# Kernel optimization log

Hardware: AMD Instinct MI355X
Metric: run time of the kernel (lower is better)

Reference implementation:

```python
import jax, jax.numpy as jnp
import numpy as np


def _knn_gather(x, idx):
    # x: (B,N,D), idx: (B,N,K) -> (B,N,K,D)
    return jax.vmap(lambda xb, ib: xb[ib])(x, idx)


def _frames_and_knn(points, k):
    # brute-force self-KNN (ascending distance; idx[...,0] == self point)
    d2 = jnp.sum(points * points, -1)
    dist = d2[:, :, None] - 2.0 * jnp.einsum('bnd,bmd->bnm', points, points) + d2[:, None, :]
    _, idx = jax.lax.top_k(-dist, k)
    knn = _knn_gather(points, idx)                       # (B,N,K,3)
    cent = knn - knn.mean(-2, keepdims=True)
    # NOTE: original divides by shape[-1]-1 == 2 (coordinate dim), faithful to source
    covs = jnp.einsum('bnki,bnkj->bnij', cent, cent) / 2.0
    _, evecs = jnp.linalg.eigh(covs)
    frames = jnp.swapaxes(evecs, -1, -2)                 # rows = eigvecs, ascending eigval
    det = jnp.linalg.det(frames)                         # det of frames BEFORE modification
    frames = frames.at[:, :, 1, :].multiply(det[..., None])
    return idx, knn, frames


def reference(points, k, local_W):
    B, N, _ = points.shape
    idx, knn, frames = _frames_and_knn(points, k)
    diff = knn - points[:, :, None, :]                   # (B,N,K,3)
    normals = frames[:, :, 0, :]
    t1 = frames[:, :, 1, :]
    t2 = frames[:, :, 2, :]
    dt = jnp.stack([jnp.einsum('bnkd,bnd->bnk', diff, t1),
                    jnp.einsum('bnkd,bnd->bnk', diff, t2)], -1)  # (B,N,K,2)

    # ---- local Voronoi area via tangent-plane grid (nested KNN, K=1) ----
    rescale = 1.1
    bbox_min = dt.min(-2) * rescale                      # (B,N,2)
    bbox_max = dt.max(-2) * rescale
    max_len = (bbox_max - bbox_min).max(-1)              # (B,N)
    coords = (dt - bbox_min[:, :, None, :]) / max_len[:, :, None, None] * 2.0 - 1.0

    lin = jnp.linspace(-1.0, 1.0, local_W, dtype=points.dtype)
    X, Y = jnp.meshgrid(lin, lin, indexing='ij')
    grid = jnp.stack([X, Y], -1).reshape(-1, 2)          # (G,2), G = local_W**2

    CHUNK = 128
    c = coords.reshape(-1, k, 2)
    n_pts = c.shape[0]
    pad = (-n_pts) % CHUNK
    c = jnp.pad(c, ((0, pad), (0, 0), (0, 0)))

    def count_fn(cc):                                    # cc: (CHUNK,K,2)
        d = jnp.sum((grid[None, :, None, :] - cc[:, None, :, :]) ** 2, -1)  # (CHUNK,G,K)
        return jnp.sum(jnp.argmin(d, -1) == 0, -1)       # grid cells owned by center

    counts = jax.lax.map(count_fn, c.reshape(-1, CHUNK, k, 2)).reshape(-1)[:n_pts]
    counts = counts.reshape(B, N).astype(points.dtype)
    voronoi_area = counts * max_len ** 2 / (local_W - 1) ** 2    # (B,N)

    # ---- Weingarten fields / Gaussian curvature ----
    ln = _knn_gather(normals, idx) - normals[:, :, None, :]      # (B,N,K,3)
    dn = jnp.stack([jnp.einsum('bnkd,bnd->bnk', ln, t1),
                    jnp.einsum('bnkd,bnd->bnk', ln, t2)], -1)    # (B,N,K,2)
    XXT = jnp.einsum('bnki,bnkj->bnij', dt, dt)                  # (B,N,2,2)
    YXT = jnp.einsum('bnki,bnkj->bnij', dn, dt)
    S = YXT + jnp.swapaxes(YXT, -1, -2)                          # YXT + XYT
    w, Q = jnp.linalg.eigh(XXT)
    QTSQ = jnp.einsum('bnji,bnjk,bnkl->bnil', Q, S, Q)           # Q^T S Q
    a, b = w[..., 0], w[..., 1]
    cmat = jnp.stack([jnp.stack([2 * a, a + b], -1),
                      jnp.stack([a + b, 2 * b], -1)], -2)        # (B,N,2,2)
    E = QTSQ / (cmat + 1e-8)
    Wmap = jnp.einsum('bnij,bnjk,bnlk->bnil', Q, E, Q)           # Q E Q^T
    gauss = jnp.linalg.det(Wmap)                                 # (B,N)

    euler = jnp.sum(gauss.reshape(-1) * voronoi_area.reshape(-1)) / 2.0 / jnp.pi
    return euler


def setup_inputs() -> dict:
    key = jax.random.key(0)
    points = jax.random.normal(key, (1, 4096, 3), dtype=jnp.float32)
    return {"points": points, "k": 50, "local_W": 64}
```

## Files before the change

kernel.cpp:

```cpp
#include <hip/hip_runtime.h>
#include <math.h>

#define NPTS 4096
#define KNB  50
#define WGRID 64

__device__ int   g_idx[NPTS * KNB];
__device__ float g_dt[NPTS * KNB * 2];
__device__ float g_nrm[NPTS * 3];
__device__ float g_t1[NPTS * 3];
__device__ float g_t2[NPTS * 3];
__device__ float g_bmin[NPTS * 2];
__device__ float g_ml[NPTS];
__device__ float g_va[NPTS];

__device__ __forceinline__ float slapy2f(float x, float y) {
  float ax = fabsf(x), ay = fabsf(y);
  float w = fmaxf(ax, ay), z = fminf(ax, ay);
  if (z == 0.0f) return w;
  float t = z / w;
  return w * sqrtf(1.0f + t * t);
}

__device__ __forceinline__ void slartgf(float f, float g, float* cs, float* sn, float* r) {
  const float safmin = 1.1754944e-38f;
  const float safmax = 8.5070592e+37f;
  const float rtmin = 1.0842022e-19f;
  const float rtmax = 6.5219496e+18f;
  if (g == 0.0f) {
    *cs = 1.0f; *sn = 0.0f; *r = f;
  } else if (f == 0.0f) {
    *cs = 0.0f; *sn = copysignf(1.0f, g); *r = fabsf(g);
  } else {
    float f1 = fabsf(f), g1 = fabsf(g);
    if (f1 > rtmin && f1 < rtmax && g1 > rtmin && g1 < rtmax) {
      float d = sqrtf(f * f + g * g);
      float p = 1.0f / d;
      *cs = f1 * p;
      *sn = g * copysignf(p, f);
      *r = copysignf(d, f);
    } else {
      float u = fminf(safmax, fmaxf(safmin, fmaxf(f1, g1)));
      float fs = f / u, gs = g / u;
      float d = sqrtf(fs * fs + gs * gs);
      float p = 1.0f / d;
      *cs = fabsf(fs) * p;
      *sn = gs * copysignf(p, f);
      *r = copysignf(d, f) * u;
    }
  }
}

__device__ void slaev2f(float a, float b, float c, float* rt1, float* rt2,
                        float* cs1, float* sn1) {
  float sm = a + c;
  float df = a - c;
  float adf = fabsf(df);
  float tb = b + b;
  float ab = fabsf(tb);
  float acmx, acmn;
  if (fabsf(a) > fabsf(c)) { acmx = a; acmn = c; } else { acmx = c; acmn = a; }
  float rt;
  if (adf > ab)      { float t = ab / adf; rt = adf * sqrtf(1.0f + t * t); }
  else if (adf < ab) { float t = adf / ab; rt = ab * sqrtf(1.0f + t * t); }
  else               { rt = ab * sqrtf(2.0f); }
  int sgn1;
  if (sm < 0.0f) {
    *rt1 = 0.5f * (sm - rt); sgn1 = -1;
    *rt2 = (acmx / *rt1) * acmn - (b / *rt1) * b;
  } else if (sm > 0.0f) {
    *rt1 = 0.5f * (sm + rt); sgn1 = 1;
    *rt2 = (acmx / *rt1) * acmn - (b / *rt1) * b;
  } else {
    *rt1 = 0.5f * rt; *rt2 = -0.5f * rt; sgn1 = 1;
  }
  float cs; int sgn2;
  if (df >= 0.0f) { cs = df + rt; sgn2 = 1; }
  else            { cs = df - rt; sgn2 = -1; }
  float acs = fabsf(cs);
  if (acs > ab) {
    float ct = -tb / cs;
    *sn1 = 1.0f / sqrtf(1.0f + ct * ct);
    *cs1 = ct * (*sn1);
  } else {
    if (ab == 0.0f) { *cs1 = 1.0f; *sn1 = 0.0f; }
    else {
      float tn = -cs / tb;
      *cs1 = 1.0f / sqrtf(1.0f + tn * tn);
      *sn1 = tn * (*cs1);
    }
  }
  if (sgn1 == sgn2) { float tn = *cs1; *cs1 = -(*sn1); *sn1 = tn; }
}

__device__ void ssteqr3(float* d, float* e, float Z[3][3]) {
  const float eps = 5.9604645e-08f;
  const float eps2 = 3.5527137e-15f;
  const float safmin = 1.1754944e-38f;
  const float ssfmax = 3.0744574e+18f;
  const float ssfmin = 3.0517578e-05f;
  const int n = 3, nmaxit = 90;
  int jtot = 0;
  for (int r = 0; r < 3; ++r)
    for (int c = 0; c < 3; ++c) Z[r][c] = (r == c) ? 1.0f : 0.0f;

  int l1 = 1;
  while (l1 <= n) {
    if (l1 > 1) e[l1 - 2] = 0.0f;
    int m = n;
    for (int mm = l1; mm <= n - 1; ++mm) {
      float tst = fabsf(e[mm - 1]);
      if (tst == 0.0f) { m = mm; break; }
      if (tst <= (sqrtf(fabsf(d[mm - 1])) * sqrtf(fabsf(d[mm]))) * eps) {
        e[mm - 1] = 0.0f; m = mm; break;
      }
    }
    int l = l1, lsv = l1, lend = m, lendsv = m;
    l1 = m + 1;
    if (lend == l) continue;

    float anorm = 0.0f;
    for (int ii = l; ii <= lend; ++ii) anorm = fmaxf(anorm, fabsf(d[ii - 1]));
    for (int ii = l; ii <= lend - 1; ++ii) anorm = fmaxf(anorm, fabsf(e[ii - 1]));
    if (anorm == 0.0f) continue;
    int iscale = 0;
    if (anorm > ssfmax) {
      iscale = 1; float mul = ssfmax / anorm;
      for (int ii = l; ii <= lend; ++ii) d[ii - 1] *= mul;
      for (int ii = l; ii <= lend - 1; ++ii) e[ii - 1] *= mul;
    } else if (anorm < ssfmin) {
      iscale = 2; float mul = ssfmin / anorm;
      for (int ii = l; ii <= lend; ++ii) d[ii - 1] *= mul;
      for (int ii = l; ii <= lend - 1; ++ii) e[ii - 1] *= mul;
    }
    if (fabsf(d[lend - 1]) < fabsf(d[l - 1])) { lend = lsv; l = lendsv; }

    if (lend > l) {
      for (;;) {
        int mm = lend;
        if (l != lend) {
          for (int t = l; t <= lend - 1; ++t) {
            float tst = e[t - 1] * e[t - 1];
            if (tst <= (eps2 * fabsf(d[t - 1])) * fabsf(d[t]) + safmin) { mm = t; break; }
          }
        }
        if (mm < lend) e[mm - 1] = 0.0f;
        float p = d[l - 1];
        if (mm == l) {
          d[l - 1] = p; ++l;
          if (l <= lend) continue; break;
        }
        if (mm == l + 1) {
          float rt1, rt2, c, s;
          slaev2f(d[l - 1], e[l - 1], d[l], &rt1, &rt2, &c, &s);
          for (int r = 0; r < 3; ++r) {
            float t = Z[r][l];
            Z[r][l]     = c * t - s * Z[r][l - 1];
            Z[r][l - 1] = s * t + c * Z[r][l - 1];
          }
          d[l - 1] = rt1; d[l] = rt2; e[l - 1] = 0.0f;
          l += 2;
          if (l <= lend) continue; break;
        }
        if (jtot == nmaxit) break;
        ++jtot;
        float g = (d[l] - p) / (2.0f * e[l - 1]);
        float r = slapy2f(g, 1.0f);
        g = d[mm - 1] - p + e[l - 1] / (g + copysignf(r, g));
        float s = 1.0f, c = 1.0f;
        p = 0.0f;
        float cw[2], sw[2];
        for (int i = mm - 1; i >= l; --i) {
          float f = s * e[i - 1];
          float b = c * e[i - 1];
          slartgf(g, f, &c, &s, &r);
          if (i != mm - 1) e[i] = r;
          g = d[i] - p;
          r = (d[i - 1] - g) * s + 2.0f * c * b;
          p = s * r;
          d[i] = g + p;
          g = c * r - b;
          cw[i - l] = c; sw[i - l] = -s;
        }
        for (int j = mm - 1; j >= l; --j) {
          float cc = cw[j - l], ss = sw[j - l];
          for (int r2 = 0; r2 < 3; ++r2) {
            float t = Z[r2][j];
            Z[r2][j]     = cc * t - ss * Z[r2][j - 1];
            Z[r2][j - 1] = ss * t + cc * Z[r2][j - 1];
          }
        }
        d[l - 1] -= p;
        e[l - 1] = g;
      }
    } else {
      for (;;) {
        int mm = lend;
        if (l != lend) {
          for (int t = l; t >= lend + 1; --t) {
            float tst = e[t - 2] * e[t - 2];
            if (tst <= (eps2 * fabsf(d[t - 1])) * fabsf(d[t - 2]) + safmin) { mm = t; break; }
          }
        }
        if (mm > lend) e[mm - 2] = 0.0f;
        float p = d[l - 1];
        if (mm == l) {
          d[l - 1] = p; --l;
          if (l >= lend) continue; break;
        }
        if (mm == l - 1) {
          float rt1, rt2, c, s;
          slaev2f(d[l - 2], e[l - 2], d[l - 1], &rt1, &rt2, &c, &s);
          for (int r2 = 0; r2 < 3; ++r2) {
            float t = Z[r2][l - 1];
            Z[r2][l - 1] = c * t - s * Z[r2][l - 2];
            Z[r2][l - 2] = s * t + c * Z[r2][l - 2];
          }
          d[l - 2] = rt1; d[l - 1] = rt2; e[l - 2] = 0.0f;
          l -= 2;
          if (l >= lend) continue; break;
        }
        if (jtot == nmaxit) break;
        ++jtot;
        float g = (d[l - 2] - p) / (2.0f * e[l - 2]);
        float r = slapy2f(g, 1.0f);
        g = d[mm - 1] - p + e[l - 2] / (g + copysignf(r, g));
        float s = 1.0f, c = 1.0f;
        p = 0.0f;
        float cw[2], sw[2];
        for (int i = mm; i <= l - 1; ++i) {
          float f = s * e[i - 1];
          float b = c * e[i - 1];
          slartgf(g, f, &c, &s, &r);
          if (i != mm) e[i - 2] = r;
          g = d[i - 1] - p;
          r = (d[i] - g) * s + 2.0f * c * b;
          p = s * r;
          d[i - 1] = g + p;
          g = c * r - b;
          cw[i - mm] = c; sw[i - mm] = s;
        }
        for (int j = mm; j <= l - 1; ++j) {
          float cc = cw[j - mm], ss = sw[j - mm];
          for (int r2 = 0; r2 < 3; ++r2) {
            float t = Z[r2][j];
            Z[r2][j]     = cc * t - ss * Z[r2][j - 1];
            Z[r2][j - 1] = ss * t + cc * Z[r2][j - 1];
          }
        }
        d[l - 1] -= p;
        e[l - 2] = g;
      }
    }
    if (iscale == 1) {
      float mul = anorm / ssfmax;
      for (int ii = lsv; ii <= lendsv; ++ii) d[ii - 1] *= mul;
      for (int ii = lsv; ii <= lendsv - 1; ++ii) e[ii - 1] *= mul;
    } else if (iscale == 2) {
      float mul = anorm / ssfmin;
      for (int ii = lsv; ii <= lendsv; ++ii) d[ii - 1] *= mul;
      for (int ii = lsv; ii <= lendsv - 1; ++ii) e[ii - 1] *= mul;
    }
    if (jtot >= nmaxit) break;
  }
  for (int ii = 2; ii <= n; ++ii) {
    int i0 = ii - 1, k0 = i0;
    float p = d[i0 - 1];
    for (int j = ii; j <= n; ++j)
      if (d[j - 1] < p) { k0 = j; p = d[j - 1]; }
    if (k0 != i0) {
      d[k0 - 1] = d[i0 - 1]; d[i0 - 1] = p;
      for (int r2 = 0; r2 < 3; ++r2) {
        float t = Z[r2][i0 - 1]; Z[r2][i0 - 1] = Z[r2][k0 - 1]; Z[r2][k0 - 1] = t;
      }
    }
  }
}

__device__ void ssytrd3(float a11, float a21, float a31, float a22, float a32, float a33,
                        float d[3], float e[2], float* tau, float* u) {
  float xnorm = fabsf(a31);
  if (xnorm == 0.0f) {
    *tau = 0.0f; *u = 0.0f;
    d[0] = a11; d[1] = a22; d[2] = a33; e[0] = a21; e[1] = a32;
    return;
  }
  float beta = -copysignf(slapy2f(a21, xnorm), a21);
  float taui = (beta - a21) / beta;
  float uu = a31 * (1.0f / (a21 - beta));
  float w1 = taui * a22 + taui * (a32 * uu);
  float w2 = taui * a32 + (taui * uu) * a33;
  float alpha = -0.5f * taui * (w1 + w2 * uu);
  w1 += alpha; w2 += alpha * uu;
  float na22 = a22 - 2.0f * w1;
  float na32 = a32 - (uu * w1 + w2);
  float na33 = a33 - 2.0f * (uu * w2);
  d[0] = a11; d[1] = na22; d[2] = na33;
  e[0] = beta; e[1] = na32;
  *tau = taui; *u = uu;
}

__global__ __launch_bounds__(256) void knn_kernel(const float* __restrict__ pts,
                                                  float* __restrict__ out, int N) {
  __shared__ unsigned skey[NPTS];
  __shared__ unsigned hist[256];
  __shared__ unsigned sred[4];
  __shared__ unsigned sbin[2];
  __shared__ int   eqi[64];
  __shared__ float eqd[64];
  __shared__ unsigned eqn[1];
  const int i = blockIdx.x;
  const int tid = threadIdx.x;
  const int lane = tid & 63, wid = tid >> 6;
  if (i == 0 && tid == 0) out[0] = 0.0f;
  const float xi = pts[3 * i], yi = pts[3 * i + 1], zi = pts[3 * i + 2];
  const float d2i = xi * xi + yi * yi + zi * zi;
  hist[tid] = 0;
  if (tid == 0) eqn[0] = 0;
  __syncthreads();
  for (int j = tid; j < N; j += 256) {
    float xj = pts[3 * j], yj = pts[3 * j + 1], zj = pts[3 * j + 2];
    float d2j = xj * xj + yj * yj + zj * zj;
    float dot = fmaf(zi, zj, fmaf(yi, yj, xi * xj));
    float dist = (d2i - 2.0f * dot) + d2j;
    float dc = fminf(fmaxf(dist, 0.0f), 31.0f);
    unsigned u = (unsigned)(dc * 134217728.0f);
    skey[j] = u;
    atomicAdd(&hist[u >> 24], 1u);
  }
  __syncthreads();
  unsigned prefix = 0, rank = 49;
  for (int pass = 0; pass < 2; ++pass) {
    const int shift = 24 - 8 * pass;
    if (pass) {
      for (int j = tid; j < N; j += 256) {
        unsigned u = skey[j];
        if ((u >> 24) == (prefix >> 24))
          atomicAdd(&hist[(u >> 16) & 255u], 1u);
      }
      __syncthreads();
    }
    unsigned h = hist[tid];
    unsigned c = h;
    #pragma unroll
    for (int off = 1; off < 64; off <<= 1) {
      unsigned o = __shfl_up(c, off);
      if (lane >= off) c += o;
    }
    if (lane == 63) sred[wid] = c;
    __syncthreads();
    unsigned wbase = 0;
    for (int w2 = 0; w2 < wid; ++w2) wbase += sred[w2];
    c += wbase;
    unsigned excl = c - h;
    if (rank >= excl && rank < c) { sbin[0] = (unsigned)tid; sbin[1] = rank - excl; }
    __syncthreads();
    prefix |= sbin[0] << shift;
    rank = sbin[1];
    __syncthreads();
    if (pass == 0) { hist[tid] = 0; __syncthreads(); }
  }
  const unsigned T = prefix;
  int cnt = 0;
  for (int j = tid; j < N; j += 256) {
    unsigned u = skey[j];
    if (u < T && j != i) {
      ++cnt;
    } else if ((u & 0xFFFF0000u) == T) {
      float xj = pts[3 * j], yj = pts[3 * j + 1], zj = pts[3 * j + 2];
      float d2j = xj * xj + yj * yj + zj * zj;
      float dot = fmaf(zi, zj, fmaf(yi, yj, xi * xj));
      float dist = (d2i - 2.0f * dot) + d2j;
      unsigned e = atomicAdd(&eqn[0], 1u);
      if (e < 64u) { eqi[e] = j; eqd[e] = dist; }
    }
  }
  __syncthreads();
  unsigned cc = (unsigned)cnt;
  #pragma unroll
  for (int off = 1; off < 64; off <<= 1) {
    unsigned o = __shfl_up(cc, off);
    if (lane >= off) cc += o;
  }
  if (lane == 63) sred[wid] = cc;
  __syncthreads();
  unsigned wbase = 0;
  for (int w2 = 0; w2 < wid; ++w2) wbase += sred[w2];
  int base = 1 + (int)(wbase + cc - (unsigned)cnt);
  for (int j = tid; j < N; j += 256) {
    unsigned u = skey[j];
    if (u < T && j != i) g_idx[i * KNB + (base++)] = j;
  }
  if (tid == 0) {
    g_idx[i * KNB] = i;
    int slot = 1 + (int)(sred[0] + sred[1] + sred[2] + sred[3]);
    int need = KNB - slot;
    int ne = (int)eqn[0]; if (ne > 64) ne = 64;
    for (int e2 = 0; e2 < need; ++e2) {
      int bq = 0, bidx = 0x7FFFFFFF; float bd = 3.4e38f;
      for (int q = 0; q < ne; ++q) {
        if (eqi[q] < 0) continue;
        float dq = eqd[q];
        if (dq < bd || (dq == bd && eqi[q] < bidx)) { bd = dq; bidx = eqi[q]; bq = q; }
      }
      g_idx[i * KNB + slot + e2] = bidx;
      eqi[bq] = -1;
    }
  }
}

__global__ __launch_bounds__(256) void frames_kernel(const float* __restrict__ pts, int N) {
  __shared__ float sx[4][52], sy[4][52], sz[4][52];
  const int tid = threadIdx.x, lane = tid & 63, w = tid >> 6;
  const int i = blockIdx.x * 4 + w;
  const int base = i * KNB;
  if (lane < KNB) {
    int j = g_idx[base + lane];
    sx[w][lane] = pts[3 * j];
    sy[w][lane] = pts[3 * j + 1];
    sz[w][lane] = pts[3 * j + 2];
  }
  __syncthreads();
  float mx = 0.0f, my = 0.0f, mz = 0.0f;
  for (int kk = 0; kk < KNB; ++kk) { mx += sx[w][kk]; my += sy[w][kk]; mz += sz[w][kk]; }
  mx /= 50.0f; my /= 50.0f; mz /= 50.0f;
  float c00 = 0, c01 = 0, c02 = 0, c11 = 0, c12 = 0, c22 = 0;
  for (int kk = 0; kk < KNB; ++kk) {
    float cx = sx[w][kk] - mx, cy = sy[w][kk] - my, cz = sz[w][kk] - mz;
    c00 = fmaf(cx, cx, c00); c01 = fmaf(cx, cy, c01); c02 = fmaf(cx, cz, c02);
    c11 = fmaf(cy, cy, c11); c12 = fmaf(cy, cz, c12); c22 = fmaf(cz, cz, c22);
  }
  c00 *= 0.5f; c01 *= 0.5f; c02 *= 0.5f; c11 *= 0.5f; c12 *= 0.5f; c22 *= 0.5f;

  float d[3], e[2], tau, u;
  ssytrd3(c00, c01, c02, c11, c12, c22, d, e, &tau, &u);
  float Z[3][3];
  ssteqr3(d, e, Z);
  if (tau != 0.0f) {
    for (int c = 0; c < 3; ++c) {
      float sum = Z[1][c] + u * Z[2][c];
      Z[1][c] -= tau * sum;
      Z[2][c] -= tau * u * sum;
    }
  }
  float n0 = Z[0][0], n1 = Z[1][0], n2 = Z[2][0];
  float a0 = Z[0][1], a1 = Z[1][1], a2 = Z[2][1];
  float b0 = Z[0][2], b1 = Z[1][2], b2 = Z[2][2];
  float cxp = a1 * b2 - a2 * b1, cyp = a2 * b0 - a0 * b2, czp = a0 * b1 - a1 * b0;
  float det = n0 * cxp + n1 * cyp + n2 * czp;
  a0 *= det; a1 *= det; a2 *= det;

  const float xi = pts[3 * i], yi = pts[3 * i + 1], zi = pts[3 * i + 2];
  float dt0 = 0.0f, dt1 = 0.0f;
  float mn0 = 3.0e38f, mx0 = -3.0e38f, mn1 = 3.0e38f, mx1 = -3.0e38f;
  if (lane < KNB) {
    float dx = sx[w][lane] - xi, dy = sy[w][lane] - yi, dz = sz[w][lane] - zi;
    dt0 = dx * a0 + dy * a1 + dz * a2;
    dt1 = dx * b0 + dy * b1 + dz * b2;
    g_dt[2 * (base + lane)] = dt0;
    g_dt[2 * (base + lane) + 1] = dt1;
    mn0 = dt0; mx0 = dt0; mn1 = dt1; mx1 = dt1;
  }
  #pragma unroll
  for (int off = 32; off > 0; off >>= 1) {
    mn0 = fminf(mn0, __shfl_down(mn0, off));
    mx0 = fmaxf(mx0, __shfl_down(mx0, off));
    mn1 = fminf(mn1, __shfl_down(mn1, off));
    mx1 = fmaxf(mx1, __shfl_down(mx1, off));
  }
  if (lane == 0) {
    g_nrm[3 * i] = n0; g_nrm[3 * i + 1] = n1; g_nrm[3 * i + 2] = n2;
    g_t1[3 * i] = a0;  g_t1[3 * i + 1] = a1;  g_t1[3 * i + 2] = a2;
    g_t2[3 * i] = b0;  g_t2[3 * i + 1] = b1;  g_t2[3 * i + 2] = b2;
    float bmin0 = mn0 * 1.1f, bmax0 = mx0 * 1.1f;
    float bmin1 = mn1 * 1.1f, bmax1 = mx1 * 1.1f;
    float ml = fmaxf(bmax0 - bmin0, bmax1 - bmin1);
    g_bmin[2 * i] = bmin0; g_bmin[2 * i + 1] = bmin1;
    g_ml[i] = ml;
  }
}

__global__ __launch_bounds__(256, 8) void voronoi_kernel(int N) {
  __shared__ float2 sc[KNB];
  __shared__ int alist[64];
  __shared__ int acnt[1];
  __shared__ int swc[4];
  const int i = blockIdx.x;
  const int tid = threadIdx.x;
  const int lane = tid & 63, wid = tid >> 6;
  const float ml = g_ml[i];
  const float b0 = g_bmin[2 * i], b1 = g_bmin[2 * i + 1];
  if (tid < KNB) {
    float dt0 = g_dt[2 * (i * KNB + tid)];
    float dt1 = g_dt[2 * (i * KNB + tid) + 1];
    sc[tid] = make_float2((dt0 - b0) / ml * 2.0f - 1.0f,
                          (dt1 - b1) / ml * 2.0f - 1.0f);
  }
  if (tid == 0) acnt[0] = 0;
  __syncthreads();
  const float step = 2.0f / 63.0f;
  if (tid < 64) {
    const int bx = tid & 7, by = tid >> 3;
    const float gx0 = fmaf((float)(bx * 8), step, -1.0f);
    const float gx1 = fmaf((float)(bx * 8 + 7), step, -1.0f);
    const float gy0 = fmaf((float)(by * 8), step, -1.0f);
    const float gy1 = fmaf((float)(by * 8 + 7), step, -1.0f);
    const float s0x = sc[0].x, s0y = sc[0].y;
    const float n0s = s0x * s0x + s0y * s0y;
    bool dead = false;
    #pragma clang loop unroll(disable)
    for (int j = 1; j < KNB && !dead; ++j) {
      float sx = sc[j].x, sy = sc[j].y;
      float ax2 = 2.0f * (sx - s0x), ay2 = 2.0f * (sy - s0y);
      float cst = n0s - (sx * sx + sy * sy);
      float Lmin = fminf(ax2 * gx0, ax2 * gx1) + fminf(ay2 * gy0, ay2 * gy1) + cst;
      dead = Lmin > 1e-4f;
    }
    if (!dead) { int p = atomicAdd(&acnt[0], 1); alist[p] = tid; }
  }
  __syncthreads();
  const int na = acnt[0];
  const float c0x = sc[0].x, c0y = sc[0].y;
  int cnt = 0;
  #pragma clang loop unroll(disable)
  for (int k = wid; k < na; k += 4) {
    int b = alist[k];
    int ix = (b & 7) * 8 + (lane & 7);
    int iy = (b >> 3) * 8 + (lane >> 3);
    float gx = fmaf((float)ix, step, -1.0f);
    float gy = fmaf((float)iy, step, -1.0f);
    float ex = gx - c0x, ey = gy - c0y;
    float d0 = ex * ex + ey * ey;
    float m = 3.0e38f;
    #pragma clang loop unroll(disable)
    for (int j = 1; j < KNB; ++j) {
      float dx = gx - sc[j].x, dy = gy - sc[j].y;
      float dd = fmaf(dx, dx, dy * dy);
      m = fminf(m, dd);
    }
    cnt += (d0 <= m) ? 1 : 0;
  }
  #pragma unroll
  for (int off = 32; off > 0; off >>= 1) cnt += __shfl_down(cnt, off);
  if (lane == 0) swc[wid] = cnt;
  __syncthreads();
  if (tid == 0) {
    int tot = swc[0] + swc[1] + swc[2] + swc[3];
    g_va[i] = (float)tot * (ml * ml) / 3969.0f;
  }
}

__global__ __launch_bounds__(256) void curv_kernel(float* __restrict__ out, int N) {
  __shared__ float s0[4][52], s1[4][52], tx[4][52], ty[4][52], tz[4][52];
  __shared__ float bsum[4];
  const int tid = threadIdx.x, lane = tid & 63, w = tid >> 6;
  const int i = blockIdx.x * 4 + w;
  const int base = i * KNB;
  if (lane < KNB) {
    int j = g_idx[base + lane];
    s0[w][lane] = g_dt[2 * (base + lane)];
    s1[w][lane] = g_dt[2 * (base + lane) + 1];
    tx[w][lane] = g_nrm[3 * j];
    ty[w][lane] = g_nrm[3 * j + 1];
    tz[w][lane] = g_nrm[3 * j + 2];
  }
  __syncthreads();
  float nx = g_nrm[3 * i], ny = g_nrm[3 * i + 1], nz = g_nrm[3 * i + 2];
  float ax = g_t1[3 * i], ay = g_t1[3 * i + 1], az = g_t1[3 * i + 2];
  float bx = g_t2[3 * i], by = g_t2[3 * i + 1], bz = g_t2[3 * i + 2];
  float xx = 0, xy = 0, yy = 0;
  float y00 = 0, y01 = 0, y10 = 0, y11 = 0;
  for (int kk = 0; kk < KNB; ++kk) {
    float dt0 = s0[w][kk], dt1 = s1[w][kk];
    float lx = tx[w][kk] - nx, ly = ty[w][kk] - ny, lz = tz[w][kk] - nz;
    float dn0 = lx * ax + ly * ay + lz * az;
    float dn1 = lx * bx + ly * by + lz * bz;
    xx = fmaf(dt0, dt0, xx); xy = fmaf(dt0, dt1, xy); yy = fmaf(dt1, dt1, yy);
    y00 = fmaf(dn0, dt0, y00); y01 = fmaf(dn0, dt1, y01);
    y10 = fmaf(dn1, dt0, y10); y11 = fmaf(dn1, dt1, y11);
  }
  float s00 = y00 + y00, s01 = y01 + y10, s11 = y11 + y11;
  float rt1, rt2, cs1, sn1;
  slaev2f(xx, xy, yy, &rt1, &rt2, &cs1, &sn1);
  float a, bb, q00, q10, q01, q11;
  if (rt1 <= rt2) { a = rt1; bb = rt2; q00 = cs1; q10 = sn1; q01 = -sn1; q11 = cs1; }
  else            { a = rt2; bb = rt1; q00 = -sn1; q10 = cs1; q01 = cs1; q11 = sn1; }
  float t00 = s00 * q00 + s01 * q10, t01 = s00 * q01 + s01 * q11;
  float t10 = s01 * q00 + s11 * q10, t11 = s01 * q01 + s11 * q11;
  float m00 = q00 * t00 + q10 * t10;
  float m01 = q00 * t01 + q10 * t11;
  float m10 = q01 * t00 + q11 * t10;
  float m11 = q01 * t01 + q11 * t11;
  float e00 = m00 / (2.0f * a + 1e-8f);
  float e01 = m01 / ((a + bb) + 1e-8f);
  float e10 = m10 / ((a + bb) + 1e-8f);
  float e11 = m11 / (2.0f * bb + 1e-8f);
  float u00 = q00 * e00 + q01 * e10, u01 = q00 * e01 + q01 * e11;
  float u10 = q10 * e00 + q11 * e10, u11 = q10 * e01 + q11 * e11;
  float w00 = u00 * q00 + u01 * q01;
  float w01 = u00 * q10 + u01 * q11;
  float w10 = u10 * q00 + u11 * q01;
  float w11 = u10 * q10 + u11 * q11;
  float gauss = w00 * w11 - w01 * w10;
  if (lane == 0) bsum[w] = gauss * g_va[i] * 0.15915494309189535f;
  __syncthreads();
  if (tid == 0)
    atomicAdd(out, bsum[0] + bsum[1] + bsum[2] + bsum[3]);
}

extern "C" void kernel_launch(void* const* d_in, const int* in_sizes, int n_in,
                              void* d_out, int out_size, void* d_ws, size_t ws_size,
                              hipStream_t stream) {
  const float* pts = (const float*)d_in[0];
  float* out = (float*)d_out;
  const int N = in_sizes[0] / 3;
  knn_kernel<<<N, 256, 0, stream>>>(pts, out, N);
  frames_kernel<<<N / 4, 256, 0, stream>>>(pts, N);
  voronoi_kernel<<<N, 256, 0, stream>>>(N);
  curv_kernel<<<N / 4, 256, 0, stream>>>(out, N);
}
```

Baseline: 166.9 us.

## Process two query points per KNN block with packed 16-bit keys and per-wave histograms

Result: slower. 173.3 us (+3.8%).

```diff
diff --git a/kernel.cpp b/kernel.cpp
--- a/kernel.cpp
+++ b/kernel.cpp
@@ -303,44 +303,42 @@
 __global__ __launch_bounds__(256) void knn_kernel(const float* __restrict__ pts,
                                                   float* __restrict__ out, int N) {
   __shared__ unsigned skey[NPTS];
-  __shared__ unsigned hist[256];
+  __shared__ unsigned whist[2][4][256];
   __shared__ unsigned sred[4];
   __shared__ unsigned sbin[2];
-  __shared__ int   eqi[64];
-  __shared__ float eqd[64];
-  __shared__ unsigned eqn[1];
-  const int i = blockIdx.x;
+  __shared__ int   eqi[2][64];
+  __shared__ float eqd[2][64];
+  __shared__ unsigned eqn[2];
   const int tid = threadIdx.x;
   const int lane = tid & 63, wid = tid >> 6;
-  if (i == 0 && tid == 0) out[0] = 0.0f;
-  const float xi = pts[3 * i], yi = pts[3 * i + 1], zi = pts[3 * i + 2];
-  const float d2i = xi * xi + yi * yi + zi * zi;
-  hist[tid] = 0;
-  if (tid == 0) eqn[0] = 0;
+  const int iA = 2 * blockIdx.x, iB = 2 * blockIdx.x + 1;
+  if (blockIdx.x == 0 && tid == 0) out[0] = 0.0f;
+  const float xiA = pts[3 * iA], yiA = pts[3 * iA + 1], ziA = pts[3 * iA + 2];
+  const float xiB = pts[3 * iB], yiB = pts[3 * iB + 1], ziB = pts[3 * iB + 2];
+  const float d2iA = xiA * xiA + yiA * yiA + ziA * ziA;
+  const float d2iB = xiB * xiB + yiB * yiB + ziB * ziB;
+  for (int b = tid; b < 2048; b += 256) ((unsigned*)whist)[b] = 0;
+  if (tid < 2) eqn[tid] = 0;
   __syncthreads();
   for (int j = tid; j < N; j += 256) {
     float xj = pts[3 * j], yj = pts[3 * j + 1], zj = pts[3 * j + 2];
     float d2j = xj * xj + yj * yj + zj * zj;
-    float dot = fmaf(zi, zj, fmaf(yi, yj, xi * xj));
-    float dist = (d2i - 2.0f * dot) + d2j;
-    float dc = fminf(fmaxf(dist, 0.0f), 31.0f);
-    unsigned u = (unsigned)(dc * 134217728.0f);
-    skey[j] = u;
-    atomicAdd(&hist[u >> 24], 1u);
-  }
-  __syncthreads();
-  unsigned prefix = 0, rank = 49;
-  for (int pass = 0; pass < 2; ++pass) {
-    const int shift = 24 - 8 * pass;
-    if (pass) {
-      for (int j = tid; j < N; j += 256) {
-        unsigned u = skey[j];
-        if ((u >> 24) == (prefix >> 24))
-          atomicAdd(&hist[(u >> 16) & 255u], 1u);
-      }
-      __syncthreads();
-    }
-    unsigned h = hist[tid];
+    float dotA = fmaf(ziA, zj, fmaf(yiA, yj, xiA * xj));
+    float distA = (d2iA - 2.0f * dotA) + d2j;
+    float dcA = fminf(fmaxf(distA, 0.0f), 31.0f);
+    unsigned kA = ((unsigned)(dcA * 134217728.0f)) >> 16;
+    float dotB = fmaf(ziB, zj, fmaf(yiB, yj, xiB * xj));
+    float distB = (d2iB - 2.0f * dotB) + d2j;
+    float dcB = fminf(fmaxf(distB, 0.0f), 31.0f);
+    unsigned kB = ((unsigned)(dcB * 134217728.0f)) >> 16;
+    skey[j] = (kA << 16) | kB;
+    atomicAdd(&whist[0][wid][kA >> 8], 1u);
+    atomicAdd(&whist[1][wid][kA >= 0 ? (kB >> 8) : 0], 1u);
+  }
+  __syncthreads();
+  unsigned b8[2], rnk[2];
+  for (int q = 0; q < 2; ++q) {
+    unsigned h = whist[q][0][tid] + whist[q][1][tid] + whist[q][2][tid] + whist[q][3][tid];
     unsigned c = h;
     #pragma unroll
     for (int off = 1; off < 64; off <<= 1) {
@@ -353,58 +351,107 @@
     for (int w2 = 0; w2 < wid; ++w2) wbase += sred[w2];
     c += wbase;
     unsigned excl = c - h;
-    if (rank >= excl && rank < c) { sbin[0] = (unsigned)tid; sbin[1] = rank - excl; }
-    __syncthreads();
-    prefix |= sbin[0] << shift;
-    rank = sbin[1];
-    __syncthreads();
-    if (pass == 0) { hist[tid] = 0; __syncthreads(); }
-  }
-  const unsigned T = prefix;
-  int cnt = 0;
+    if (49u >= excl && 49u < c) { sbin[0] = (unsigned)tid; sbin[1] = 49u - excl; }
+    __syncthreads();
+    b8[q] = sbin[0]; rnk[q] = sbin[1];
+    __syncthreads();
+  }
+  for (int b = tid; b < 2048; b += 256) ((unsigned*)whist)[b] = 0;
+  __syncthreads();
   for (int j = tid; j < N; j += 256) {
-    unsigned u = skey[j];
-    if (u < T && j != i) {
-      ++cnt;
-    } else if ((u & 0xFFFF0000u) == T) {
+    unsigned k = skey[j];
+    unsigned kA = k >> 16, kB = k & 0xFFFFu;
+    if ((kA >> 8) == b8[0]) atomicAdd(&whist[0][wid][kA & 255u], 1u);
+    if ((kB >> 8) == b8[1]) atomicAdd(&whist[1][wid][kB & 255u], 1u);
+  }
+  __syncthreads();
+  unsigned T16[2];
+  for (int q = 0; q < 2; ++q) {
+    unsigned h = whist[q][0][tid] + whist[q][1][tid] + whist[q][2][tid] + whist[q][3][tid];
+    unsigned c = h;
+    #pragma unroll
+    for (int off = 1; off < 64; off <<= 1) {
+      unsigned o = __shfl_up(c, off);
+      if (lane >= off) c += o;
+    }
+    if (lane == 63) sred[wid] = c;
+    __syncthreads();
+    unsigned wbase = 0;
+    for (int w2 = 0; w2 < wid; ++w2) wbase += sred[w2];
+    c += wbase;
+    unsigned excl = c - h;
+    unsigned r = rnk[q];
+    if (r >= excl && r < c) { sbin[0] = (unsigned)tid; }
+    __syncthreads();
+    T16[q] = (b8[q] << 8) | sbin[0];
+    __syncthreads();
+  }
+  int cntA = 0, cntB = 0;
+  for (int j = tid; j < N; j += 256) {
+    unsigned k = skey[j];
+    unsigned kA = k >> 16, kB = k & 0xFFFFu;
+    if (kA < T16[0] && j != iA) {
+      ++cntA;
+    } else if (kA == T16[0]) {
       float xj = pts[3 * j], yj = pts[3 * j + 1], zj = pts[3 * j + 2];
       float d2j = xj * xj + yj * yj + zj * zj;
-      float dot = fmaf(zi, zj, fmaf(yi, yj, xi * xj));
-      float dist = (d2i - 2.0f * dot) + d2j;
+      float dot = fmaf(ziA, zj, fmaf(yiA, yj, xiA * xj));
+      float dist = (d2iA - 2.0f * dot) + d2j;
       unsigned e = atomicAdd(&eqn[0], 1u);
-      if (e < 64u) { eqi[e] = j; eqd[e] = dist; }
-    }
-  }
-  __syncthreads();
-  unsigned cc = (unsigned)cnt;
-  #pragma unroll
-  for (int off = 1; off < 64; off <<= 1) {
-    unsigned o = __shfl_up(cc, off);
-    if (lane >= off) cc += o;
-  }
-  if (lane == 63) sred[wid] = cc;
-  __syncthreads();
-  unsigned wbase = 0;
-  for (int w2 = 0; w2 < wid; ++w2) wbase += sred[w2];
-  int base = 1 + (int)(wbase + cc - (unsigned)cnt);
+      if (e < 64u) { eqi[0][e] = j; eqd[0][e] = dist; }
+    }
+    if (kB < T16[1] && j != iB) {
+      ++cntB;
+    } else if (kB == T16[1]) {
+      float xj = pts[3 * j], yj = pts[3 * j + 1], zj = pts[3 * j + 2];
+      float d2j = xj * xj + yj * yj + zj * zj;
+      float dot = fmaf(ziB, zj, fmaf(yiB, yj, xiB * xj));
+      float dist = (d2iB - 2.0f * dot) + d2j;
+      unsigned e = atomicAdd(&eqn[1], 1u);
+      if (e < 64u) { eqi[1][e] = j; eqd[1][e] = dist; }
+    }
+  }
+  __syncthreads();
+  int baseq[2], slotq[2];
+  for (int q = 0; q < 2; ++q) {
+    unsigned cc = (unsigned)(q == 0 ? cntA : cntB);
+    unsigned mine = cc;
+    #pragma unroll
+    for (int off = 1; off < 64; off <<= 1) {
+      unsigned o = __shfl_up(cc, off);
+      if (lane >= off) cc += o;
+    }
+    if (lane == 63) sred[wid] = cc;
+    __syncthreads();
+    unsigned wbase = 0;
+    for (int w2 = 0; w2 < wid; ++w2) wbase += sred[w2];
+    baseq[q] = 1 + (int)(wbase + cc - mine);
+    slotq[q] = 1 + (int)(sred[0] + sred[1] + sred[2] + sred[3]);
+    __syncthreads();
+  }
+  int bA = baseq[0], bB = baseq[1];
   for (int j = tid; j < N; j += 256) {
-    unsigned u = skey[j];
-    if (u < T && j != i) g_idx[i * KNB + (base++)] = j;
+    unsigned k = skey[j];
+    if ((k >> 16) < T16[0] && j != iA) g_idx[iA * KNB + (bA++)] = j;
+    if ((k & 0xFFFFu) < T16[1] && j != iB) g_idx[iB * KNB + (bB++)] = j;
   }
   if (tid == 0) {
-    g_idx[i * KNB] = i;
-    int slot = 1 + (int)(sred[0] + sred[1] + sred[2] + sred[3]);
-    int need = KNB - slot;
-    int ne = (int)eqn[0]; if (ne > 64) ne = 64;
-    for (int e2 = 0; e2 < need; ++e2) {
-      int bq = 0, bidx = 0x7FFFFFFF; float bd = 3.4e38f;
-      for (int q = 0; q < ne; ++q) {
-        if (eqi[q] < 0) continue;
-        float dq = eqd[q];
-        if (dq < bd || (dq == bd && eqi[q] < bidx)) { bd = dq; bidx = eqi[q]; bq = q; }
+    for (int q = 0; q < 2; ++q) {
+      int iq = (q == 0) ? iA : iB;
+      g_idx[iq * KNB] = iq;
+      int slot = slotq[q];
+      int need = KNB - slot;
+      int ne = (int)eqn[q]; if (ne > 64) ne = 64;
+      for (int e2 = 0; e2 < need; ++e2) {
+        int bq = 0, bidx = 0x7FFFFFFF; float bd = 3.4e38f;
+        for (int qq = 0; qq < ne; ++qq) {
+          if (eqi[q][qq] < 0) continue;
+          float dq = eqd[q][qq];
+          if (dq < bd || (dq == bd && eqi[q][qq] < bidx)) { bd = dq; bidx = eqi[q][qq]; bq = qq; }
+        }
+        g_idx[iq * KNB + slot + e2] = bidx;
+        eqi[q][bq] = -1;
       }
-      g_idx[i * KNB + slot + e2] = bidx;
-      eqi[bq] = -1;
     }
   }
 }
@@ -614,7 +661,7 @@
   const float* pts = (const float*)d_in[0];
   float* out = (float*)d_out;
   const int N = in_sizes[0] / 3;
-  knn_kernel<<<N, 256, 0, stream>>>(pts, out, N);
+  knn_kernel<<<N / 2, 256, 0, stream>>>(pts, out, N);
   frames_kernel<<<N / 4, 256, 0, stream>>>(pts, N);
   voronoi_kernel<<<N, 256, 0, stream>>>(N);
   curv_kernel<<<N / 4, 256, 0, stream>>>(out, N);
```
